# Optimization experiments

Measured on AMD Instinct MI355X. Metric: run time of the kernel, lower is better.

## Reference

```python
import jax, jax.numpy as jnp
import numpy as np

DIM, E, K = 256, 8, 2
B, D, H, W = 1, 32, 32, 32
EPS = 1e-5


def setup_inputs() -> dict:
    key = jax.random.key(0)
    ks = jax.random.split(key, 16)
    nrm = lambda k, s, sc=0.02: jax.random.normal(k, s, jnp.float32) * sc
    def resblock_params(k):
        k1, k2, k3, k4 = jax.random.split(k, 4)
        return dict(
            c1w=nrm(k1, (DIM, DIM, 3, 3, 3)), c1b=jnp.zeros((DIM,), jnp.float32),
            g1=jax.random.uniform(k2, (DIM,), jnp.float32, 0.5, 1.5), be1=jnp.zeros((DIM,), jnp.float32),
            c2w=nrm(k3, (DIM, DIM, 3, 3, 3)), c2b=jnp.zeros((DIM,), jnp.float32),
            g2=jax.random.uniform(k4, (DIM,), jnp.float32, 0.5, 1.5), be2=jnp.zeros((DIM,), jnp.float32),
        )
    p1 = resblock_params(ks[5])
    p2 = resblock_params(ks[6])
    return {
        "x": jax.random.normal(ks[0], (B, DIM, D, H, W), jnp.float32),
        "wg": nrm(ks[1], (DIM, E)),
        "w1": nrm(ks[2], (E, DIM, DIM)), "b1": jnp.zeros((E, DIM), jnp.float32),
        "w2": nrm(ks[3], (E, DIM, DIM)), "b2": jnp.zeros((E, DIM), jnp.float32),
        "r1_c1w": p1["c1w"], "r1_c1b": p1["c1b"], "r1_g1": p1["g1"], "r1_be1": p1["be1"],
        "r1_c2w": p1["c2w"], "r1_c2b": p1["c2b"], "r1_g2": p1["g2"], "r1_be2": p1["be2"],
        "r2_c1w": p2["c1w"], "r2_c1b": p2["c1b"], "r2_g1": p2["g1"], "r2_be1": p2["be1"],
        "r2_c2w": p2["c2w"], "r2_c2b": p2["c2b"], "r2_g2": p2["g2"], "r2_be2": p2["be2"],
        "c8w": nrm(ks[4], (DIM, DIM, 1, 1, 1)), "c8b": jnp.zeros((DIM,), jnp.float32),
    }


def conv3d(x, w, b, pad):
    y = jax.lax.conv_general_dilated(
        x, w, window_strides=(1, 1, 1), padding=[(pad, pad)] * 3,
        dimension_numbers=("NCDHW", "OIDHW", "NCDHW"))
    return y + b[None, :, None, None, None]


def batchnorm(x, g, b):
    m = x.mean(axis=(0, 2, 3, 4), keepdims=True)
    v = x.var(axis=(0, 2, 3, 4), keepdims=True)
    return g[None, :, None, None, None] * (x - m) * jax.lax.rsqrt(v + EPS) + b[None, :, None, None, None]


def unet_res_block(x, c1w, c1b, g1, be1, c2w, c2b, g2, be2):
    out = jax.nn.leaky_relu(batchnorm(conv3d(x, c1w, c1b, 1), g1, be1), 0.01)
    out = batchnorm(conv3d(out, c2w, c2b, 1), g2, be2)
    return jax.nn.leaky_relu(out + x, 0.01)  # identity shortcut (in==out ch, stride 1)


def mom_block(x, wg, w1, b1, w2, b2):
    Bb, C, Dd, Hh, Ww = x.shape
    tokens = x.transpose(0, 2, 3, 4, 1).reshape(-1, C)  # [T, C]
    T = tokens.shape[0]
    probs = jax.nn.softmax(tokens @ wg, axis=-1)          # [T, E]
    vals, idx = jax.lax.top_k(probs, K)                   # [T, K]
    wts = vals / vals.sum(-1, keepdims=True)
    gates = jnp.zeros((T, E), probs.dtype).at[jnp.arange(T)[:, None], idx].set(wts)
    # dense expert MLPs (math-equivalent to gather/dispatch/combine)
    h = jax.nn.gelu(jnp.einsum("tc,ech->eth", tokens, w1) + b1[:, None, :])
    eo = jnp.einsum("eth,ehc->etc", h, w2) + b2[:, None, :]
    moe = jnp.einsum("te,etc->tc", gates, eo)             # [T, C]
    # switch-style load-balancing auxiliary loss
    density = (gates > 0).astype(probs.dtype).mean(0)     # fraction of tokens per expert
    density_proxy = probs.mean(0)
    aux = (density * density_proxy).sum() * E
    out = x + moe.reshape(Bb, Dd, Hh, Ww, C).transpose(0, 4, 1, 2, 3)
    return out, aux


def reference(x, wg, w1, b1, w2, b2,
              r1_c1w, r1_c1b, r1_g1, r1_be1, r1_c2w, r1_c2b, r1_g2, r1_be2,
              r2_c1w, r2_c1b, r2_g1, r2_be1, r2_c2w, r2_c2b, r2_g2, r2_be2,
              c8w, c8b):
    xm, aux = mom_block(x, wg, w1, b1, w2, b2)
    res = unet_res_block(xm, r1_c1w, r1_c1b, r1_g1, r1_be1, r1_c2w, r1_c2b, r1_g2, r1_be2)
    res = unet_res_block(res, r2_c1w, r2_c1b, r2_g1, r2_be1, r2_c2w, r2_c2b, r2_g2, r2_be2)
    out = xm + conv3d(res, c8w, c8b, 0)  # Dropout3d is identity at eval
    return out, aux
```

## Files before the change

### kernel.cpp

```cpp
#include <hip/hip_runtime.h>
#include <stdint.h>

typedef __attribute__((ext_vector_type(8))) short short8;
typedef __attribute__((ext_vector_type(4))) float f32x4;
typedef unsigned short u16;
typedef unsigned int u32;
typedef unsigned long long u64;

#define WS_TOK   0ull
#define WS_XT    16777216ull
#define WS_XMCT  50331648ull
#define WS_GATES 83886080ull
#define WS_H     84934656ull
#define WS_P1    135266304ull
#define WS_P2    155389952ull
#define WS_Y     175513600ull
#define WS_R2    209068032ull
#define WS_WRB   225845248ull
#define WS_W1P   240001024ull
#define WS_W2P   241049600ull
#define WS_C8P   242098176ull
#define WS_PART  242229248ull
#define WS_SF    243277824ull
#define WS_AUXP  243279872ull

#define WS_PERM  (WS_H + 0x00000ull)
#define WS_TBL   (WS_H + 0x60000ull)
#define WS_META  (WS_H + 0x70000ull)
#define WS_BCNT  (WS_H + 0x80000ull)
#define WS_BOFF  (WS_H + 0x90000ull)
#define WS_SEL   (WS_H + 0x100000ull)

__device__ __forceinline__ u16 f2bf(float f) {
  u32 x = __float_as_uint(f);
  u32 r = x + 0x7fffu + ((x >> 16) & 1u);
  return (u16)(r >> 16);
}
__device__ __forceinline__ float bf2f(u32 u) { return __uint_as_float(u << 16); }

__global__ void trans_in_k(const float* __restrict__ x, float* __restrict__ xt,
                           u16* __restrict__ tok) {
  __shared__ float ld[64][65];
  int tt = blockIdx.x, cc = blockIdx.y, tid = threadIdx.x;
#pragma unroll
  for (int k = 0; k < 16; ++k) {
    int idx = tid + k * 256;
    int cl = idx >> 6, j = idx & 63;
    ld[cl][j] = x[(size_t)(cc * 64 + cl) * 32768 + tt * 64 + j];
  }
  __syncthreads();
#pragma unroll
  for (int k = 0; k < 16; ++k) {
    int idx = tid + k * 256;
    int tl = idx >> 6, cl = idx & 63;
    float v = ld[cl][tl];
    size_t o = (size_t)(tt * 64 + tl) * 256 + cc * 64 + cl;
    xt[o] = v;
    tok[o] = f2bf(v);
  }
}

__global__ void pack_rb_k(const float* __restrict__ w0, const float* __restrict__ w1,
                          const float* __restrict__ w2, const float* __restrict__ w3,
                          u16* __restrict__ out) {
  __shared__ float ld[6912];
  int conv = blockIdx.x >> 8, blk = blockIdx.x & 255, tid = threadIdx.x;
  const float* src = conv == 0 ? w0 : conv == 1 ? w1 : conv == 2 ? w2 : w3;
  size_t base = (size_t)blk * 256 * 27;
#pragma unroll
  for (int k = 0; k < 27; ++k) ld[tid + k * 256] = src[base + tid + k * 256];
  __syncthreads();
  u16* dst = out + (size_t)conv * 27 * 65536;
  int n = blk * 256 + tid;
#pragma unroll
  for (int tap = 0; tap < 27; ++tap)
    dst[(size_t)tap * 65536 + n] = f2bf(ld[tid * 27 + tap]);
}

__global__ void pack_tr_k(const float* __restrict__ w1, const float* __restrict__ w2,
                          u16* __restrict__ w1p, u16* __restrict__ w2p) {
  __shared__ float ld[64][65];
  int m = blockIdx.y, tile = blockIdx.x, tid = threadIdx.x;
  const float* src = (m < 8) ? (w1 + (size_t)m * 65536) : (w2 + (size_t)(m - 8) * 65536);
  u16* dst = (m < 8) ? (w1p + (size_t)m * 65536) : (w2p + (size_t)(m - 8) * 65536);
  int r0 = (tile >> 2) * 64, c0 = (tile & 3) * 64;
#pragma unroll
  for (int k = 0; k < 16; ++k) {
    int idx = tid + k * 256;
    int rr = idx >> 6, cc = idx & 63;
    ld[rr][cc] = src[(size_t)(r0 + rr) * 256 + c0 + cc];
  }
  __syncthreads();
#pragma unroll
  for (int k = 0; k < 16; ++k) {
    int idx = tid + k * 256;
    int cc = idx >> 6, rr = idx & 63;
    dst[(size_t)(c0 + cc) * 256 + r0 + rr] = f2bf(ld[rr][cc]);
  }
}

__global__ void cvt_k(const float* __restrict__ in, u16* __restrict__ out, int n) {
  int i = blockIdx.x * 256 + threadIdx.x;
  if (i < n) out[i] = f2bf(in[i]);
}

__global__ void halo_k(u16* __restrict__ P1, u16* __restrict__ P2) {
  int gid = blockIdx.x * 256 + threadIdx.x;
  int r = gid >> 5, o = (gid & 31) << 3;
  if (r >= 39304) return;
  int d = r / 1156, rem = r - d * 1156, h = rem / 34, w = rem - h * 34;
  if (d >= 1 && d <= 32 && h >= 1 && h <= 32 && w >= 1 && w <= 32) return;
  uint4 z = {0u, 0u, 0u, 0u};
  *(uint4*)(P1 + (size_t)r * 256 + o) = z;
  *(uint4*)(P2 + (size_t)r * 256 + o) = z;
}

__global__ void gate_k(const float* __restrict__ xt, const float* __restrict__ wg,
                       float* __restrict__ gw, u32* __restrict__ sel,
                       u32* __restrict__ blk_cnt, float* __restrict__ auxp) {
  __shared__ float wgs[2048];
  __shared__ float ax[4][16];
  __shared__ u32 bc[4][8];
  int tid = threadIdx.x;
#pragma unroll
  for (int k = 0; k < 8; ++k) wgs[tid + k * 256] = wg[tid + k * 256];
  __syncthreads();
  int t = blockIdx.x * 256 + tid;
  int lane = tid & 63, wv = tid >> 6;
  float l[8] = {0, 0, 0, 0, 0, 0, 0, 0};
  const float* xr = xt + (size_t)t * 256;
  for (int c = 0; c < 256; c += 4) {
    float4 xv = *(const float4*)(xr + c);
#pragma unroll
    for (int e = 0; e < 8; ++e)
      l[e] += xv.x * wgs[c * 8 + e] + xv.y * wgs[(c + 1) * 8 + e] +
              xv.z * wgs[(c + 2) * 8 + e] + xv.w * wgs[(c + 3) * 8 + e];
  }
  float mx = l[0];
#pragma unroll
  for (int e = 1; e < 8; ++e) mx = fmaxf(mx, l[e]);
  float p[8], sum = 0.f;
#pragma unroll
  for (int e = 0; e < 8; ++e) { p[e] = __expf(l[e] - mx); sum += p[e]; }
  float inv = 1.0f / sum;
#pragma unroll
  for (int e = 0; e < 8; ++e) p[e] *= inv;
  int i0 = 0; float v0 = p[0];
#pragma unroll
  for (int e = 1; e < 8; ++e) if (p[e] > v0) { v0 = p[e]; i0 = e; }
  int i1 = -1; float v1 = -1.0f;
#pragma unroll
  for (int e = 0; e < 8; ++e) if (e != i0 && p[e] > v1) { v1 = p[e]; i1 = e; }
  float wsum = v0 + v1;
  gw[t * 2] = v0 / wsum;
  gw[t * 2 + 1] = v1 / wsum;
  sel[t] = (u32)i0 | ((u32)i1 << 4);
  u64 mm[8];
#pragma unroll
  for (int e = 0; e < 8; ++e) mm[e] = __ballot(i0 == e || i1 == e);
  if (lane == 0) {
#pragma unroll
    for (int e = 0; e < 8; ++e) bc[wv][e] = (u32)__popcll(mm[e]);
  }
#pragma unroll
  for (int e = 0; e < 8; ++e) {
    float ps = p[e];
    float cn = (e == i0 || e == i1) ? 1.0f : 0.0f;
    for (int o = 32; o; o >>= 1) { ps += __shfl_down(ps, o); cn += __shfl_down(cn, o); }
    if (lane == 0) { ax[wv][e] = ps; ax[wv][8 + e] = cn; }
  }
  __syncthreads();
  if (tid < 16)
    auxp[blockIdx.x * 16 + tid] = ax[0][tid] + ax[1][tid] + ax[2][tid] + ax[3][tid];
  if (tid < 8)
    blk_cnt[blockIdx.x * 8 + tid] = bc[0][tid] + bc[1][tid] + bc[2][tid] + bc[3][tid];
}

__global__ void aux_k(const float* __restrict__ auxp, float* __restrict__ out) {
  __shared__ float s[16];
  int i = threadIdx.x;
  if (i < 16) {
    float a = 0;
    for (int b = 0; b < 128; ++b) a += auxp[b * 16 + i];
    s[i] = a;
  }
  __syncthreads();
  if (i == 0) {
    float r = 0;
    for (int e = 0; e < 8; ++e)
      r += (s[8 + e] * (1.0f / 32768.0f)) * (s[e] * (1.0f / 32768.0f));
    out[0] = r * 8.0f;
  }
}

__global__ void scan_k(const u32* __restrict__ blk_cnt, u32* __restrict__ blkoff,
                       u32* __restrict__ tbl, u32* __restrict__ meta,
                       u32* __restrict__ perm) {
  __shared__ u32 tot[8], base[8], nck[8], cbase[8];
  int tid = threadIdx.x;
  if (tid < 8) {
    u32 run = 0;
    for (int b = 0; b < 128; ++b) {
      blkoff[b * 8 + tid] = run;
      run += blk_cnt[b * 8 + tid];
    }
    tot[tid] = run;
  }
  __syncthreads();
  if (tid == 0) {
    u32 acc = 0, c = 0;
    for (int e = 0; e < 8; ++e) {
      base[e] = acc;
      u32 nc = (tot[e] + 127) >> 7;
      nck[e] = nc;
      cbase[e] = c;
      acc += nc << 7;
      c += nc;
    }
    meta[0] = c;
  }
  __syncthreads();
  for (int i = tid; i < 1024; i += 256) blkoff[i] += base[i & 7];
  if (tid < 8) {
    for (u32 k = 0; k < nck[tid]; ++k)
      tbl[cbase[tid] + k] = ((base[tid] + (k << 7)) << 4) | (u32)tid;
    for (u32 sl = base[tid] + tot[tid]; sl < base[tid] + (nck[tid] << 7); ++sl)
      perm[sl] = 0;
  }
}

__global__ void scatter_k(const u32* __restrict__ sel, const u32* __restrict__ blkoff,
                          u32* __restrict__ perm, u32* __restrict__ tpos) {
  __shared__ u32 wcnt[4][8];
  int tid = threadIdx.x, b = blockIdx.x;
  int lane = tid & 63, wv = tid >> 6;
  int t = b * 256 + tid;
  u32 s = sel[t];
  int i0 = s & 15, i1 = (s >> 4) & 15;
  u64 mm[8];
#pragma unroll
  for (int e = 0; e < 8; ++e) mm[e] = __ballot(i0 == e || i1 == e);
  if (lane == 0) {
#pragma unroll
    for (int e = 0; e < 8; ++e) wcnt[wv][e] = (u32)__popcll(mm[e]);
  }
  __syncthreads();
  u64 lt = (1ull << lane) - 1ull;
#pragma unroll
  for (int e = 0; e < 8; ++e) {
    bool is0 = (i0 == e), is1 = (i1 == e);
    if (is0 || is1) {
      u32 woff = 0;
#pragma unroll
      for (int w = 0; w < 4; ++w)
        if (w < wv) woff += wcnt[w][e];
      u32 pos = blkoff[b * 8 + e] + woff + (u32)__popcll(mm[e] & lt);
      perm[pos] = (u32)t;
      tpos[t * 2 + (is0 ? 0 : 1)] = pos;
    }
  }
}

__global__ __launch_bounds__(512, 2) void moe_gemm_k(
    const u16* __restrict__ tok, const u32* __restrict__ perm,
    const u32* __restrict__ tbl, const u32* __restrict__ meta,
    const u16* __restrict__ w1p, const u16* __restrict__ w2p,
    const float* __restrict__ b1, const float* __restrict__ b2,
    u16* __restrict__ eo) {
  __shared__ __attribute__((aligned(16))) unsigned char smem[163840];
  const int bid = blockIdx.x;
  if ((u32)bid >= meta[0]) return;
  const u32 ent = tbl[bid];
  const int e = (int)(ent & 15u);
  const int slot0 = (int)(ent >> 4);
  const int tid = threadIdx.x;
  const int lane = tid & 63;
  const int wv = tid >> 6;
  const int wr = (wv >> 2) * 64;
  const int wc = (wv & 3) * 64;
  const int fq = lane >> 4, fr = lane & 15;
  const u16* w1e = w1p + e * 65536;
  const u16* w2e = w2p + e * 65536;

#pragma unroll
  for (int it = 0; it < 8; ++it) {
    int s = tid + it * 512;
    int r = s >> 5, seg = s & 31;
    int cole = ((seg >> 3) << 6) + (((seg & 7) ^ (r & 7)) << 3);
    u32 rowtok = perm[slot0 + r];
    __builtin_amdgcn_global_load_lds(
        (const __attribute__((address_space(1))) u32*)(tok + (size_t)rowtok * 256 + cole),
        (__attribute__((address_space(3))) u32*)(smem + s * 16), 16, 0, 0);
  }

  f32x4 acc1[4][4];
#pragma unroll
  for (int mc = 0; mc < 4; ++mc)
#pragma unroll
    for (int nt = 0; nt < 4; ++nt) acc1[mc][nt] = (f32x4){0.f, 0.f, 0.f, 0.f};

#pragma unroll 1
  for (int kc = 0; kc < 4; ++kc) {
#pragma unroll
    for (int it = 0; it < 4; ++it) {
      int s = tid + it * 512;
      int r = s >> 3;
      int sub = (s & 7) ^ (r & 7);
      __builtin_amdgcn_global_load_lds(
          (const __attribute__((address_space(1))) u32*)(w1e + (size_t)r * 256 + kc * 64 + sub * 8),
          (__attribute__((address_space(3))) u32*)(smem + 65536 + s * 16), 16, 0, 0);
    }
    __syncthreads();
#pragma unroll
    for (int khf = 0; khf < 2; ++khf) {
      short8 af1[4], bt[4];
#pragma unroll
      for (int mc = 0; mc < 4; ++mc) {
        int row = wc + mc * 16 + fr;
        int p = (khf * 4 + fq) ^ (row & 7);
        af1[mc] = *(const short8*)(smem + 65536 + row * 128 + p * 16);
      }
#pragma unroll
      for (int nt = 0; nt < 4; ++nt) {
        int row = wr + nt * 16 + fr;
        int p = (khf * 4 + fq) ^ (row & 7);
        bt[nt] = *(const short8*)(smem + row * 512 + kc * 128 + p * 16);
      }
#pragma unroll
      for (int mc = 0; mc < 4; ++mc)
#pragma unroll
        for (int nt = 0; nt < 4; ++nt)
          acc1[mc][nt] = __builtin_amdgcn_mfma_f32_16x16x32_bf16(af1[mc], bt[nt], acc1[mc][nt], 0, 0, 0);
    }
    __syncthreads();
  }

#pragma unroll
  for (int mc = 0; mc < 4; ++mc) {
    int k0 = wc + mc * 16 + fq * 4;
    float4 bv = *(const float4*)(b1 + e * 256 + k0);
#pragma unroll
    for (int nt = 0; nt < 4; ++nt) {
      int t = wr + nt * 16 + fr;
      u64 pk = 0;
#pragma unroll
      for (int j = 0; j < 4; ++j) {
        float v = acc1[mc][nt][j] + ((const float*)&bv)[j];
        float u = 1.5957691216057308f * (v + 0.044715f * v * v * v);
        float g = v / (1.0f + __expf(-u));
        pk |= (u64)f2bf(g) << (16 * j);
      }
      *(u64*)(smem + 98304 + t * 512 + ((k0 * 2) ^ ((t & 7) << 4))) = pk;
    }
  }

  f32x4 acc2[4][4];
#pragma unroll
  for (int m = 0; m < 4; ++m)
#pragma unroll
    for (int n = 0; n < 4; ++n) acc2[m][n] = (f32x4){0.f, 0.f, 0.f, 0.f};

#pragma unroll 1
  for (int kc = 0; kc < 4; ++kc) {
#pragma unroll
    for (int it = 0; it < 4; ++it) {
      int s = tid + it * 512;
      int r = s >> 3;
      int sub = (s & 7) ^ (r & 7);
      __builtin_amdgcn_global_load_lds(
          (const __attribute__((address_space(1))) u32*)(w2e + (size_t)r * 256 + kc * 64 + sub * 8),
          (__attribute__((address_space(3))) u32*)(smem + 65536 + s * 16), 16, 0, 0);
    }
    __syncthreads();
#pragma unroll
    for (int khf = 0; khf < 2; ++khf) {
      short8 af[4], bb[4];
#pragma unroll
      for (int m = 0; m < 4; ++m) {
        int row = wr + m * 16 + fr;
        int col = (kc * 128 + (khf * 4 + fq) * 16) ^ ((row & 7) << 4);
        af[m] = *(const short8*)(smem + 98304 + row * 512 + col);
      }
#pragma unroll
      for (int n = 0; n < 4; ++n) {
        int row = wc + n * 16 + fr;
        int p = (khf * 4 + fq) ^ (row & 7);
        bb[n] = *(const short8*)(smem + 65536 + row * 128 + p * 16);
      }
#pragma unroll
      for (int m = 0; m < 4; ++m)
#pragma unroll
        for (int n = 0; n < 4; ++n)
          acc2[m][n] = __builtin_amdgcn_mfma_f32_16x16x32_bf16(af[m], bb[n], acc2[m][n], 0, 0, 0);
    }
    __syncthreads();
  }

  float bs2[4];
#pragma unroll
  for (int n = 0; n < 4; ++n) bs2[n] = b2[e * 256 + wc + n * 16 + fr];
#pragma unroll
  for (int m = 0; m < 4; ++m)
#pragma unroll
    for (int j = 0; j < 4; ++j) {
      int rowslot = slot0 + wr + m * 16 + fq * 4 + j;
      u16* er = eo + (size_t)rowslot * 256 + wc;
#pragma unroll
      for (int n = 0; n < 4; ++n) er[n * 16 + fr] = f2bf(acc2[m][n][j] + bs2[n]);
    }
}

__global__ void combine_k(float* __restrict__ xt, const u16* __restrict__ eo,
                          const float* __restrict__ gw, const u32* __restrict__ tpos,
                          float* __restrict__ xmct, u16* __restrict__ pad) {
  __shared__ float ld[64][65];
  __shared__ u32 pp[64][2];
  __shared__ float gg[64][2];
  int tt = blockIdx.x, cc = blockIdx.y, tid = threadIdx.x;
  if (tid < 128) {
    int tl = tid >> 1, s = tid & 1;
    int t = tt * 64 + tl;
    pp[tl][s] = tpos[t * 2 + s];
    gg[tl][s] = gw[t * 2 + s];
  }
  __syncthreads();
#pragma unroll
  for (int k = 0; k < 16; ++k) {
    int idx = tid + k * 256;
    int tl = idx >> 6, cl = idx & 63;
    int c = cc * 64 + cl;
    size_t o = (size_t)(tt * 64 + tl) * 256 + c;
    float e0 = bf2f(eo[(size_t)pp[tl][0] * 256 + c]);
    float e1 = bf2f(eo[(size_t)pp[tl][1] * 256 + c]);
    float v = xt[o] + gg[tl][0] * e0 + gg[tl][1] * e1;
    xt[o] = v;
    ld[tl][cl] = v;
    int t = tt * 64 + tl;
    int d = t >> 10, h = (t >> 5) & 31, w = t & 31;
    int prow = (d + 1) * 1156 + (h + 1) * 34 + (w + 1);
    pad[(size_t)prow * 256 + c] = f2bf(v);
  }
  __syncthreads();
#pragma unroll
  for (int k = 0; k < 16; ++k) {
    int idx = tid + k * 256;
    int cl = idx >> 6, tl = idx & 63;
    xmct[(size_t)(cc * 64 + cl) * 32768 + tt * 64 + tl] = ld[tl][cl];
  }
}

__global__ __launch_bounds__(512, 1) void conv_k(
    const u16* __restrict__ P, const u16* __restrict__ W,
    const float* __restrict__ bias, u16* __restrict__ y,
    float* __restrict__ part) {
  __shared__ __attribute__((aligned(16))) unsigned char smem[147456];
  const int tid = threadIdx.x;
  const int bx = blockIdx.x;
  const int ttile = (bx & 7) * 32 + (bx >> 3);
  const int lane = tid & 63;
  const int wv = tid >> 6;
  const int wr = (wv >> 2) << 6;
  const int wc = (wv & 3) << 6;
  const int fq = lane >> 4, fr = lane & 15;
  const int dd = ttile >> 3, h0 = (ttile & 7) << 2;

  int goffA[2];
#pragma unroll
  for (int it = 0; it < 2; ++it) {
    int s = tid + it * 512;
    int r = s >> 3, c = s & 7;
    int base = dd * 1156 + (h0 + (r >> 5)) * 34 + (r & 31);
    goffA[it] = base * 256 + ((c ^ (r & 7)) << 3);
  }
  int goffB[4];
#pragma unroll
  for (int it = 0; it < 4; ++it) {
    int s = tid + it * 512;
    int r = s >> 3, c = s & 7;
    goffB[it] = r * 256 + ((c ^ (r & 7)) << 3);
  }

  f32x4 acc[4][4];
#pragma unroll
  for (int m = 0; m < 4; ++m)
#pragma unroll
    for (int n = 0; n < 4; ++n) acc[m][n] = (f32x4){0.f, 0.f, 0.f, 0.f};

#define CONV_STAGE(s2, half)                                                        \
  {                                                                                 \
    int tap_ = (s2) >> 2, kc_ = (s2) & 3;                                           \
    int aofs_ = ((tap_ / 9) * 1156 + ((tap_ / 3) % 3) * 34 + (tap_ % 3)) * 256 +    \
                kc_ * 64;                                                           \
    int bofs_ = tap_ * 65536 + kc_ * 64;                                            \
    unsigned char* sb_ = smem + ((s2) % 3) * 49152;                                 \
    if ((half) == 0) {                                                              \
      __builtin_amdgcn_global_load_lds(                                             \
          (const __attribute__((address_space(1))) u32*)(P + aofs_ + goffA[0]),     \
          (__attribute__((address_space(3))) u32*)(sb_ + tid * 16), 16, 0, 0);      \
      __builtin_amdgcn_global_load_lds(                                             \
          (const __attribute__((address_space(1))) u32*)(P + aofs_ + goffA[1]),     \
          (__attribute__((address_space(3))) u32*)(sb_ + (tid + 512) * 16), 16, 0, 0); \
      __builtin_amdgcn_global_load_lds(                                             \
          (const __attribute__((address_space(1))) u32*)(W + bofs_ + goffB[0]),     \
          (__attribute__((address_space(3))) u32*)(sb_ + 16384 + tid * 16), 16, 0, 0); \
    } else {                                                                        \
      __builtin_amdgcn_global_load_lds(                                             \
          (const __attribute__((address_space(1))) u32*)(W + bofs_ + goffB[1]),     \
          (__attribute__((address_space(3))) u32*)(sb_ + 16384 + (tid + 512) * 16), \
          16, 0, 0);                                                                \
      __builtin_amdgcn_global_load_lds(                                             \
          (const __attribute__((address_space(1))) u32*)(W + bofs_ + goffB[2]),     \
          (__attribute__((address_space(3))) u32*)(sb_ + 16384 + (tid + 1024) * 16),\
          16, 0, 0);                                                                \
      __builtin_amdgcn_global_load_lds(                                             \
          (const __attribute__((address_space(1))) u32*)(W + bofs_ + goffB[3]),     \
          (__attribute__((address_space(3))) u32*)(sb_ + 16384 + (tid + 1536) * 16),\
          16, 0, 0);                                                                \
    }                                                                               \
  }

  CONV_STAGE(0, 0); CONV_STAGE(0, 1);
  CONV_STAGE(1, 0); CONV_STAGE(1, 1);
  asm volatile("s_waitcnt vmcnt(6)" ::: "memory");
  __builtin_amdgcn_s_barrier();

#pragma unroll 1
  for (int s = 0; s < 108; ++s) {
    const unsigned char* sb = smem + (s % 3) * 49152;
    const bool doStage = (s < 106);
#pragma unroll
    for (int khf = 0; khf < 2; ++khf) {
      short8 af[4], bb[4];
#pragma unroll
      for (int m = 0; m < 4; ++m) {
        int row = wr + m * 16 + fr;
        int p = (khf * 4 + fq) ^ (row & 7);
        af[m] = *(const short8*)(sb + row * 128 + p * 16);
      }
#pragma unroll
      for (int n = 0; n < 4; ++n) {
        int row = wc + n * 16 + fr;
        int p = (khf * 4 + fq) ^ (row & 7);
        bb[n] = *(const short8*)(sb + 16384 + row * 128 + p * 16);
      }
      if (doStage) CONV_STAGE(s + 2, khf);
      __builtin_amdgcn_s_barrier();
      __builtin_amdgcn_s_setprio(1);
#pragma unroll
      for (int m = 0; m < 4; ++m)
#pragma unroll
        for (int n = 0; n < 4; ++n)
          acc[m][n] = __builtin_amdgcn_mfma_f32_16x16x32_bf16(af[m], bb[n], acc[m][n], 0, 0, 0);
      __builtin_amdgcn_s_setprio(0);
      if (khf == 0) __builtin_amdgcn_s_barrier();
    }
    if (doStage)
      asm volatile("s_waitcnt vmcnt(6)" ::: "memory");
    else
      asm volatile("s_waitcnt vmcnt(0)" ::: "memory");
    __builtin_amdgcn_s_barrier();
  }
#undef CONV_STAGE

  float bs[4];
#pragma unroll
  for (int n = 0; n < 4; ++n) bs[n] = bias[wc + n * 16 + fr];

  float sn[4] = {0, 0, 0, 0}, qn[4] = {0, 0, 0, 0};
#pragma unroll
  for (int m = 0; m < 4; ++m) {
#pragma unroll
    for (int j = 0; j < 4; ++j) {
      int t = ttile * 128 + wr + m * 16 + fq * 4 + j;
      u16* yr = y + (size_t)t * 256 + wc;
#pragma unroll
      for (int n = 0; n < 4; ++n) {
        float v = acc[m][n][j] + bs[n];
        yr[n * 16 + fr] = f2bf(v);
        sn[n] += v;
        qn[n] += v * v;
      }
    }
  }
#pragma unroll
  for (int n = 0; n < 4; ++n) {
    float s = sn[n], q = qn[n];
    s += __shfl_xor(s, 16); s += __shfl_xor(s, 32);
    q += __shfl_xor(q, 16); q += __shfl_xor(q, 32);
    if (lane < 16) {
      int pi = (ttile * 2 + (wv >> 2)) * 256 + wc + n * 16 + fr;
      part[pi] = s;
      part[131072 + pi] = q;
    }
  }
}

__global__ __launch_bounds__(256, 2) void final_k(
    const u16* __restrict__ A, const u16* __restrict__ Bw,
    const float* __restrict__ bias, float* __restrict__ outF,
    const float* __restrict__ xmct) {
  __shared__ __attribute__((aligned(16))) unsigned char smem[65536];
  const int tid = threadIdx.x;
  const int ttile = blockIdx.x;
  const int ctile = blockIdx.y;
  const int lane = tid & 63;
  const int wv = tid >> 6;
  const int wr = (wv >> 1) << 6;
  const int wc = (wv & 1) << 6;
  const int fq = lane >> 4;
  const int fr = lane & 15;

  int aoff[4], boff[4];
#pragma unroll
  for (int it = 0; it < 4; ++it) {
    int s = tid + it * 256;
    int r = s >> 3;
    int lsg = (s & 7) ^ (r & 7);
    aoff[it] = (ttile * 128 + r) * 256 + lsg * 8;
    boff[it] = (ctile * 128 + r) * 256 + lsg * 8;
  }

  f32x4 acc[4][4];
#pragma unroll
  for (int m = 0; m < 4; ++m)
#pragma unroll
    for (int n = 0; n < 4; ++n) acc[m][n] = (f32x4){0.f, 0.f, 0.f, 0.f};

  auto stage = [&](int kc, int buf) {
    const u16* Ak = A + kc * 64;
    const u16* Bk = Bw + kc * 64;
    unsigned char* sb = smem + buf * 32768;
#pragma unroll
    for (int it = 0; it < 4; ++it) {
      __builtin_amdgcn_global_load_lds(
          (const __attribute__((address_space(1))) u32*)(Ak + aoff[it]),
          (__attribute__((address_space(3))) u32*)(sb + (tid + it * 256) * 16),
          16, 0, 0);
      __builtin_amdgcn_global_load_lds(
          (const __attribute__((address_space(1))) u32*)(Bk + boff[it]),
          (__attribute__((address_space(3))) u32*)(sb + 16384 + (tid + it * 256) * 16),
          16, 0, 0);
    }
  };
  auto compute = [&](int buf) {
    unsigned char* sb = smem + buf * 32768;
#pragma unroll
    for (int khf = 0; khf < 2; ++khf) {
      short8 af[4], bb[4];
#pragma unroll
      for (int m = 0; m < 4; ++m) {
        int row = wr + m * 16 + fr;
        int p = (khf * 4 + fq) ^ (row & 7);
        af[m] = *(const short8*)(sb + row * 128 + p * 16);
      }
#pragma unroll
      for (int n = 0; n < 4; ++n) {
        int row = wc + n * 16 + fr;
        int p = (khf * 4 + fq) ^ (row & 7);
        bb[n] = *(const short8*)(sb + 16384 + row * 128 + p * 16);
      }
#pragma unroll
      for (int m = 0; m < 4; ++m)
#pragma unroll
        for (int n = 0; n < 4; ++n)
          acc[m][n] = __builtin_amdgcn_mfma_f32_16x16x32_bf16(af[m], bb[n], acc[m][n], 0, 0, 0);
    }
  };

  stage(0, 0);
  asm volatile("s_waitcnt vmcnt(0)" ::: "memory");
  __builtin_amdgcn_s_barrier();
  int cur = 0;
#pragma unroll 1
  for (int s = 0; s < 4; ++s) {
    if (s + 1 < 4) stage(s + 1, cur ^ 1);
    compute(cur);
    asm volatile("s_waitcnt vmcnt(0)" ::: "memory");
    __builtin_amdgcn_s_barrier();
    cur ^= 1;
  }

  float bs[4];
#pragma unroll
  for (int n = 0; n < 4; ++n) bs[n] = bias[ctile * 128 + wc + n * 16 + fr];

#pragma unroll
  for (int m = 0; m < 4; ++m) {
    int trow = ttile * 128 + wr + m * 16 + fq * 4;
#pragma unroll
    for (int n = 0; n < 4; ++n) {
      int oc = ctile * 128 + wc + n * 16 + fr;
      size_t o = (size_t)oc * 32768 + trow;
      float4 xv = *(const float4*)(xmct + o);
      float4 w;
      w.x = acc[m][n][0] + bs[n] + xv.x;
      w.y = acc[m][n][1] + bs[n] + xv.y;
      w.z = acc[m][n][2] + bs[n] + xv.z;
      w.w = acc[m][n][3] + bs[n] + xv.w;
      *(float4*)(outF + o) = w;
    }
  }
}

__global__ void stats2_k(const float* __restrict__ part, const float* __restrict__ g,
                         const float* __restrict__ be, float* __restrict__ sf) {
  __shared__ float sred[4][256], qred[4][256];
  int tid = threadIdx.x;
  int c = tid & 255, qd = tid >> 8;
  float s = 0, q = 0;
  for (int b = qd * 128; b < qd * 128 + 128; ++b) {
    s += part[b * 256 + c];
    q += part[131072 + b * 256 + c];
  }
  sred[qd][c] = s;
  qred[qd][c] = q;
  __syncthreads();
  if (qd == 0) {
    s = sred[0][c] + sred[1][c] + sred[2][c] + sred[3][c];
    q = qred[0][c] + qred[1][c] + qred[2][c] + qred[3][c];
    float mean = s * (1.0f / 32768.0f);
    float var = q * (1.0f / 32768.0f) - mean * mean;
    float a = g[c] * rsqrtf(var + 1e-5f);
    sf[c] = a;
    sf[256 + c] = be[c] - mean * a;
  }
}

template <int V>
__global__ void bn_k(const u16* __restrict__ y, const float* __restrict__ sf,
                     const float* __restrict__ skip, u16* __restrict__ pad,
                     float* __restrict__ f32o, u16* __restrict__ bfo) {
  int gid = blockIdx.x * 256 + threadIdx.x;
  int t = gid >> 5, c0 = (gid & 31) << 3;
  size_t base = (size_t)t * 256 + c0;
  float v[8];
  uint4 yv = *(const uint4*)(y + base);
  v[0] = bf2f(yv.x & 0xffffu); v[1] = bf2f(yv.x >> 16);
  v[2] = bf2f(yv.y & 0xffffu); v[3] = bf2f(yv.y >> 16);
  v[4] = bf2f(yv.z & 0xffffu); v[5] = bf2f(yv.z >> 16);
  v[6] = bf2f(yv.w & 0xffffu); v[7] = bf2f(yv.w >> 16);
  const float4* ap = (const float4*)(sf + c0);
  float4 a0 = ap[0], a1 = ap[1];
  const float4* shp = (const float4*)(sf + 256 + c0);
  float4 s0 = shp[0], s1 = shp[1];
  v[0] = a0.x * v[0] + s0.x; v[1] = a0.y * v[1] + s0.y;
  v[2] = a0.z * v[2] + s0.z; v[3] = a0.w * v[3] + s0.w;
  v[4] = a1.x * v[4] + s1.x; v[5] = a1.y * v[5] + s1.y;
  v[6] = a1.z * v[6] + s1.z; v[7] = a1.w * v[7] + s1.w;
  if (V >= 1) {
    const float4* kp = (const float4*)(skip + base);
    float4 k0 = kp[0], k1 = kp[1];
    v[0] += k0.x; v[1] += k0.y; v[2] += k0.z; v[3] += k0.w;
    v[4] += k1.x; v[5] += k1.y; v[6] += k1.z; v[7] += k1.w;
  }
#pragma unroll
  for (int i = 0; i < 8; ++i) v[i] = v[i] > 0.0f ? v[i] : 0.01f * v[i];
  if (V <= 1) {
    int d = t >> 10, h = (t >> 5) & 31, w = t & 31;
    int prow = (d + 1) * 1156 + (h + 1) * 34 + (w + 1);
    uint4 pk;
    pk.x = (u32)f2bf(v[0]) | ((u32)f2bf(v[1]) << 16);
    pk.y = (u32)f2bf(v[2]) | ((u32)f2bf(v[3]) << 16);
    pk.z = (u32)f2bf(v[4]) | ((u32)f2bf(v[5]) << 16);
    pk.w = (u32)f2bf(v[6]) | ((u32)f2bf(v[7]) << 16);
    *(uint4*)(pad + (size_t)prow * 256 + c0) = pk;
  }
  if (V == 1) {
    float4 o0 = {v[0], v[1], v[2], v[3]}, o1 = {v[4], v[5], v[6], v[7]};
    float4* fp = (float4*)(f32o + base);
    fp[0] = o0; fp[1] = o1;
  }
  if (V == 2) {
    uint4 pk;
    pk.x = (u32)f2bf(v[0]) | ((u32)f2bf(v[1]) << 16);
    pk.y = (u32)f2bf(v[2]) | ((u32)f2bf(v[3]) << 16);
    pk.z = (u32)f2bf(v[4]) | ((u32)f2bf(v[5]) << 16);
    pk.w = (u32)f2bf(v[6]) | ((u32)f2bf(v[7]) << 16);
    *(uint4*)(bfo + base) = pk;
  }
}

extern "C" void kernel_launch(void* const* d_in, const int* in_sizes, int n_in,
                              void* d_out, int out_size, void* d_ws, size_t ws_size,
                              hipStream_t stream) {
  (void)in_sizes; (void)n_in; (void)out_size; (void)ws_size;
  const float* x  = (const float*)d_in[0];
  const float* wg = (const float*)d_in[1];
  const float* w1 = (const float*)d_in[2];
  const float* b1 = (const float*)d_in[3];
  const float* w2 = (const float*)d_in[4];
  const float* b2 = (const float*)d_in[5];

  char* ws = (char*)d_ws;
  u16* tok    = (u16*)(ws + WS_TOK);
  float* xt   = (float*)(ws + WS_XT);
  float* xmct = (float*)(ws + WS_XMCT);
  float* gw   = (float*)(ws + WS_GATES);
  u32* tpos   = (u32*)(ws + WS_GATES + 0x80000ull);
  u32* perm   = (u32*)(ws + WS_PERM);
  u32* tbl    = (u32*)(ws + WS_TBL);
  u32* meta   = (u32*)(ws + WS_META);
  u32* bcnt   = (u32*)(ws + WS_BCNT);
  u32* boff   = (u32*)(ws + WS_BOFF);
  u32* selb   = (u32*)(ws + WS_SEL);
  u16* P1     = (u16*)(ws + WS_P1);
  u16* P2     = (u16*)(ws + WS_P2);
  u16* ybuf   = (u16*)(ws + WS_Y);
  u16* eo     = (u16*)(ws + WS_Y);
  u16* r2b    = (u16*)(ws + WS_R2);
  u16* wrb    = (u16*)(ws + WS_WRB);
  u16* w1p    = (u16*)(ws + WS_W1P);
  u16* w2p    = (u16*)(ws + WS_W2P);
  u16* c8p    = (u16*)(ws + WS_C8P);
  float* part = (float*)(ws + WS_PART);
  float* sf   = (float*)(ws + WS_SF);
  float* auxp = (float*)(ws + WS_AUXP);
  float* outp = (float*)d_out;

  halo_k<<<4913, 256, 0, stream>>>(P1, P2);
  trans_in_k<<<dim3(512, 4), 256, 0, stream>>>(x, xt, tok);
  pack_rb_k<<<1024, 256, 0, stream>>>((const float*)d_in[6], (const float*)d_in[10],
                                      (const float*)d_in[14], (const float*)d_in[18], wrb);
  pack_tr_k<<<dim3(16, 16), 256, 0, stream>>>(w1, w2, w1p, w2p);
  cvt_k<<<256, 256, 0, stream>>>((const float*)d_in[22], c8p, 65536);

  gate_k<<<128, 256, 0, stream>>>(xt, wg, gw, selb, bcnt, auxp);
  scan_k<<<1, 256, 0, stream>>>(bcnt, boff, tbl, meta, perm);
  scatter_k<<<128, 256, 0, stream>>>(selb, boff, perm, tpos);
  moe_gemm_k<<<520, 512, 0, stream>>>(tok, perm, tbl, meta, w1p, w2p, b1, b2, eo);
  combine_k<<<dim3(512, 4), 256, 0, stream>>>(xt, eo, gw, tpos, xmct, P1);

  conv_k<<<256, 512, 0, stream>>>(P1, wrb + 0 * 1769472, (const float*)d_in[7], ybuf, part);
  stats2_k<<<1, 1024, 0, stream>>>(part, (const float*)d_in[8], (const float*)d_in[9], sf);
  bn_k<0><<<4096, 256, 0, stream>>>(ybuf, sf, nullptr, P2, nullptr, nullptr);
  conv_k<<<256, 512, 0, stream>>>(P2, wrb + 1 * 1769472, (const float*)d_in[11], ybuf, part);
  stats2_k<<<1, 1024, 0, stream>>>(part, (const float*)d_in[12], (const float*)d_in[13], sf);
  bn_k<1><<<4096, 256, 0, stream>>>(ybuf, sf, xt, P1, xt, nullptr);

  conv_k<<<256, 512, 0, stream>>>(P1, wrb + 2 * 1769472, (const float*)d_in[15], ybuf, part);
  stats2_k<<<1, 1024, 0, stream>>>(part, (const float*)d_in[16], (const float*)d_in[17], sf);
  bn_k<0><<<4096, 256, 0, stream>>>(ybuf, sf, nullptr, P2, nullptr, nullptr);
  conv_k<<<256, 512, 0, stream>>>(P2, wrb + 3 * 1769472, (const float*)d_in[19], ybuf, part);
  stats2_k<<<1, 1024, 0, stream>>>(part, (const float*)d_in[20], (const float*)d_in[21], sf);
  bn_k<2><<<4096, 256, 0, stream>>>(ybuf, sf, xt, nullptr, nullptr, r2b);

  final_k<<<dim3(256, 2), 256, 0, stream>>>(r2b, c8p, (const float*)d_in[23], outp, xmct);
  aux_k<<<1, 64, 0, stream>>>(auxp, outp + 8388608);
}
```

Measured before the change: 737.9 us.

## Double-buffer MoE weight loads, simplify conv pipeline, parallelize BN stats, gate from raw input

The MoE GEMM now double-buffers its expert-weight chunks in LDS and prefetches the next chunk while computing the current one. It also reuses the token region for the hidden activations, cutting LDS from 160KB to 128KB. The conv kernel's staged-load macro becomes lambdas that issue each stage's loads all at once, dropping the split-half staging, the mid-loop barriers and the setprio hints. stats2 runs across 16 blocks instead of one. The gate kernel reads the channel-major input directly, so it no longer depends on the transpose kernel. The conv scheduling change could lose the overlap the interleaved barriers gave, and the gate's strided reads may coalesce differently.

```diff
diff --git a/kernel.cpp b/kernel.cpp
--- a/kernel.cpp
+++ b/kernel.cpp
@@ -115,7 +115,7 @@
   *(uint4*)(P2 + (size_t)r * 256 + o) = z;
 }
 
-__global__ void gate_k(const float* __restrict__ xt, const float* __restrict__ wg,
+__global__ void gate_k(const float* __restrict__ x, const float* __restrict__ wg,
                        float* __restrict__ gw, u32* __restrict__ sel,
                        u32* __restrict__ blk_cnt, float* __restrict__ auxp) {
   __shared__ float wgs[2048];
@@ -128,13 +128,11 @@
   int t = blockIdx.x * 256 + tid;
   int lane = tid & 63, wv = tid >> 6;
   float l[8] = {0, 0, 0, 0, 0, 0, 0, 0};
-  const float* xr = xt + (size_t)t * 256;
-  for (int c = 0; c < 256; c += 4) {
-    float4 xv = *(const float4*)(xr + c);
-#pragma unroll
-    for (int e = 0; e < 8; ++e)
-      l[e] += xv.x * wgs[c * 8 + e] + xv.y * wgs[(c + 1) * 8 + e] +
-              xv.z * wgs[(c + 2) * 8 + e] + xv.w * wgs[(c + 3) * 8 + e];
+#pragma unroll 4
+  for (int c = 0; c < 256; ++c) {
+    float xv = x[(size_t)c * 32768 + t];
+#pragma unroll
+    for (int e = 0; e < 8; ++e) l[e] += xv * wgs[c * 8 + e];
   }
   float mx = l[0];
 #pragma unroll
@@ -267,7 +265,7 @@
     const u16* __restrict__ w1p, const u16* __restrict__ w2p,
     const float* __restrict__ b1, const float* __restrict__ b2,
     u16* __restrict__ eo) {
-  __shared__ __attribute__((aligned(16))) unsigned char smem[163840];
+  __shared__ __attribute__((aligned(16))) unsigned char smem[131072];
   const int bid = blockIdx.x;
   if ((u32)bid >= meta[0]) return;
   const u32 ent = tbl[bid];
@@ -282,6 +280,14 @@
   const u16* w1e = w1p + e * 65536;
   const u16* w2e = w2p + e * 65536;
 
+  int woff[4];
+#pragma unroll
+  for (int it = 0; it < 4; ++it) {
+    int s = tid + it * 512;
+    int r = s >> 3;
+    woff[it] = r * 256 + (((s & 7) ^ (r & 7)) << 3);
+  }
+
 #pragma unroll
   for (int it = 0; it < 8; ++it) {
     int s = tid + it * 512;
@@ -292,6 +298,13 @@
         (const __attribute__((address_space(1))) u32*)(tok + (size_t)rowtok * 256 + cole),
         (__attribute__((address_space(3))) u32*)(smem + s * 16), 16, 0, 0);
   }
+#pragma unroll
+  for (int it = 0; it < 4; ++it)
+    __builtin_amdgcn_global_load_lds(
+        (const __attribute__((address_space(1))) u32*)(w1e + woff[it]),
+        (__attribute__((address_space(3))) u32*)(smem + 65536 + (tid + it * 512) * 16),
+        16, 0, 0);
+  __syncthreads();
 
   f32x4 acc1[4][4];
 #pragma unroll
@@ -301,16 +314,15 @@
 
 #pragma unroll 1
   for (int kc = 0; kc < 4; ++kc) {
-#pragma unroll
-    for (int it = 0; it < 4; ++it) {
-      int s = tid + it * 512;
-      int r = s >> 3;
-      int sub = (s & 7) ^ (r & 7);
+    const u16* nw = (kc < 3) ? (w1e + (kc + 1) * 64) : w2e;
+    unsigned char* nb = smem + 65536 + (((kc + 1) & 1) * 32768);
+#pragma unroll
+    for (int it = 0; it < 4; ++it)
       __builtin_amdgcn_global_load_lds(
-          (const __attribute__((address_space(1))) u32*)(w1e + (size_t)r * 256 + kc * 64 + sub * 8),
-          (__attribute__((address_space(3))) u32*)(smem + 65536 + s * 16), 16, 0, 0);
-    }
-    __syncthreads();
+          (const __attribute__((address_space(1))) u32*)(nw + woff[it]),
+          (__attribute__((address_space(3))) u32*)(nb + (tid + it * 512) * 16),
+          16, 0, 0);
+    const unsigned char* wb = smem + 65536 + ((kc & 1) * 32768);
 #pragma unroll
     for (int khf = 0; khf < 2; ++khf) {
       short8 af1[4], bt[4];
@@ -318,7 +330,7 @@
       for (int mc = 0; mc < 4; ++mc) {
         int row = wc + mc * 16 + fr;
         int p = (khf * 4 + fq) ^ (row & 7);
-        af1[mc] = *(const short8*)(smem + 65536 + row * 128 + p * 16);
+        af1[mc] = *(const short8*)(wb + row * 128 + p * 16);
       }
 #pragma unroll
       for (int nt = 0; nt < 4; ++nt) {
@@ -350,9 +362,10 @@
         float g = v / (1.0f + __expf(-u));
         pk |= (u64)f2bf(g) << (16 * j);
       }
-      *(u64*)(smem + 98304 + t * 512 + ((k0 * 2) ^ ((t & 7) << 4))) = pk;
-    }
-  }
+      *(u64*)(smem + t * 512 + ((k0 * 2) ^ ((t & 7) << 4))) = pk;
+    }
+  }
+  __syncthreads();
 
   f32x4 acc2[4][4];
 #pragma unroll
@@ -362,16 +375,17 @@
 
 #pragma unroll 1
   for (int kc = 0; kc < 4; ++kc) {
-#pragma unroll
-    for (int it = 0; it < 4; ++it) {
-      int s = tid + it * 512;
-      int r = s >> 3;
-      int sub = (s & 7) ^ (r & 7);
-      __builtin_amdgcn_global_load_lds(
-          (const __attribute__((address_space(1))) u32*)(w2e + (size_t)r * 256 + kc * 64 + sub * 8),
-          (__attribute__((address_space(3))) u32*)(smem + 65536 + s * 16), 16, 0, 0);
-    }
-    __syncthreads();
+    if (kc < 3) {
+      unsigned char* nb = smem + 65536 + (((kc + 1) & 1) * 32768);
+      const u16* nw = w2e + (kc + 1) * 64;
+#pragma unroll
+      for (int it = 0; it < 4; ++it)
+        __builtin_amdgcn_global_load_lds(
+            (const __attribute__((address_space(1))) u32*)(nw + woff[it]),
+            (__attribute__((address_space(3))) u32*)(nb + (tid + it * 512) * 16),
+            16, 0, 0);
+    }
+    const unsigned char* wb = smem + 65536 + ((kc & 1) * 32768);
 #pragma unroll
     for (int khf = 0; khf < 2; ++khf) {
       short8 af[4], bb[4];
@@ -379,13 +393,13 @@
       for (int m = 0; m < 4; ++m) {
         int row = wr + m * 16 + fr;
         int col = (kc * 128 + (khf * 4 + fq) * 16) ^ ((row & 7) << 4);
-        af[m] = *(const short8*)(smem + 98304 + row * 512 + col);
+        af[m] = *(const short8*)(smem + row * 512 + col);
       }
 #pragma unroll
       for (int n = 0; n < 4; ++n) {
         int row = wc + n * 16 + fr;
         int p = (khf * 4 + fq) ^ (row & 7);
-        bb[n] = *(const short8*)(smem + 65536 + row * 128 + p * 16);
+        bb[n] = *(const short8*)(wb + row * 128 + p * 16);
       }
 #pragma unroll
       for (int m = 0; m < 4; ++m)
@@ -464,20 +478,20 @@
   const int fq = lane >> 4, fr = lane & 15;
   const int dd = ttile >> 3, h0 = (ttile & 7) << 2;
 
-  int goffA[2];
+  int aoff[2];
 #pragma unroll
   for (int it = 0; it < 2; ++it) {
     int s = tid + it * 512;
     int r = s >> 3, c = s & 7;
     int base = dd * 1156 + (h0 + (r >> 5)) * 34 + (r & 31);
-    goffA[it] = base * 256 + ((c ^ (r & 7)) << 3);
-  }
-  int goffB[4];
+    aoff[it] = base * 256 + ((c ^ (r & 7)) << 3);
+  }
+  int boff[4];
 #pragma unroll
   for (int it = 0; it < 4; ++it) {
     int s = tid + it * 512;
     int r = s >> 3, c = s & 7;
-    goffB[it] = r * 256 + ((c ^ (r & 7)) << 3);
+    boff[it] = r * 256 + ((c ^ (r & 7)) << 3);
   }
 
   f32x4 acc[4][4];
@@ -486,48 +500,26 @@
 #pragma unroll
     for (int n = 0; n < 4; ++n) acc[m][n] = (f32x4){0.f, 0.f, 0.f, 0.f};
 
-#define CONV_STAGE(s2, half)                                                        \
-  {                                                                                 \
-    int tap_ = (s2) >> 2, kc_ = (s2) & 3;                                           \
-    int aofs_ = ((tap_ / 9) * 1156 + ((tap_ / 3) % 3) * 34 + (tap_ % 3)) * 256 +    \
-                kc_ * 64;                                                           \
-    int bofs_ = tap_ * 65536 + kc_ * 64;                                            \
-    unsigned char* sb_ = smem + ((s2) % 3) * 49152;                                 \
-    if ((half) == 0) {                                                              \
-      __builtin_amdgcn_global_load_lds(                                             \
-          (const __attribute__((address_space(1))) u32*)(P + aofs_ + goffA[0]),     \
-          (__attribute__((address_space(3))) u32*)(sb_ + tid * 16), 16, 0, 0);      \
-      __builtin_amdgcn_global_load_lds(                                             \
-          (const __attribute__((address_space(1))) u32*)(P + aofs_ + goffA[1]),     \
-          (__attribute__((address_space(3))) u32*)(sb_ + (tid + 512) * 16), 16, 0, 0); \
-      __builtin_amdgcn_global_load_lds(                                             \
-          (const __attribute__((address_space(1))) u32*)(W + bofs_ + goffB[0]),     \
-          (__attribute__((address_space(3))) u32*)(sb_ + 16384 + tid * 16), 16, 0, 0); \
-    } else {                                                                        \
-      __builtin_amdgcn_global_load_lds(                                             \
-          (const __attribute__((address_space(1))) u32*)(W + bofs_ + goffB[1]),     \
-          (__attribute__((address_space(3))) u32*)(sb_ + 16384 + (tid + 512) * 16), \
-          16, 0, 0);                                                                \
-      __builtin_amdgcn_global_load_lds(                                             \
-          (const __attribute__((address_space(1))) u32*)(W + bofs_ + goffB[2]),     \
-          (__attribute__((address_space(3))) u32*)(sb_ + 16384 + (tid + 1024) * 16),\
-          16, 0, 0);                                                                \
-      __builtin_amdgcn_global_load_lds(                                             \
-          (const __attribute__((address_space(1))) u32*)(W + bofs_ + goffB[3]),     \
-          (__attribute__((address_space(3))) u32*)(sb_ + 16384 + (tid + 1536) * 16),\
-          16, 0, 0);                                                                \
-    }                                                                               \
-  }
-
-  CONV_STAGE(0, 0); CONV_STAGE(0, 1);
-  CONV_STAGE(1, 0); CONV_STAGE(1, 1);
-  asm volatile("s_waitcnt vmcnt(6)" ::: "memory");
-  __builtin_amdgcn_s_barrier();
-
-#pragma unroll 1
-  for (int s = 0; s < 108; ++s) {
-    const unsigned char* sb = smem + (s % 3) * 49152;
-    const bool doStage = (s < 106);
+  auto stage = [&](int s, int buf) {
+    int tap = s >> 2, kc = s & 3;
+    int aofs = ((tap / 9) * 1156 + ((tap / 3) % 3) * 34 + (tap % 3)) * 256 + kc * 64;
+    int bofs = tap * 65536 + kc * 64;
+    unsigned char* sb = smem + buf * 49152;
+#pragma unroll
+    for (int it = 0; it < 2; ++it)
+      __builtin_amdgcn_global_load_lds(
+          (const __attribute__((address_space(1))) u32*)(P + aofs + aoff[it]),
+          (__attribute__((address_space(3))) u32*)(sb + (tid + it * 512) * 16),
+          16, 0, 0);
+#pragma unroll
+    for (int it = 0; it < 4; ++it)
+      __builtin_amdgcn_global_load_lds(
+          (const __attribute__((address_space(1))) u32*)(W + bofs + boff[it]),
+          (__attribute__((address_space(3))) u32*)(sb + 16384 + (tid + it * 512) * 16),
+          16, 0, 0);
+  };
+  auto compute = [&](int buf) {
+    const unsigned char* sb = smem + buf * 49152;
 #pragma unroll
     for (int khf = 0; khf < 2; ++khf) {
       short8 af[4], bb[4];
@@ -543,24 +535,29 @@
         int p = (khf * 4 + fq) ^ (row & 7);
         bb[n] = *(const short8*)(sb + 16384 + row * 128 + p * 16);
       }
-      if (doStage) CONV_STAGE(s + 2, khf);
-      __builtin_amdgcn_s_barrier();
-      __builtin_amdgcn_s_setprio(1);
 #pragma unroll
       for (int m = 0; m < 4; ++m)
 #pragma unroll
         for (int n = 0; n < 4; ++n)
           acc[m][n] = __builtin_amdgcn_mfma_f32_16x16x32_bf16(af[m], bb[n], acc[m][n], 0, 0, 0);
-      __builtin_amdgcn_s_setprio(0);
-      if (khf == 0) __builtin_amdgcn_s_barrier();
-    }
-    if (doStage)
+    }
+  };
+
+  stage(0, 0);
+  stage(1, 1);
+  asm volatile("s_waitcnt vmcnt(6)" ::: "memory");
+  __builtin_amdgcn_s_barrier();
+
+#pragma unroll 1
+  for (int s = 0; s < 108; ++s) {
+    if (s < 106) stage(s + 2, (s + 2) % 3);
+    compute(s % 3);
+    if (s < 106)
       asm volatile("s_waitcnt vmcnt(6)" ::: "memory");
     else
       asm volatile("s_waitcnt vmcnt(0)" ::: "memory");
     __builtin_amdgcn_s_barrier();
   }
-#undef CONV_STAGE
 
   float bs[4];
 #pragma unroll
@@ -643,7 +640,7 @@
     }
   };
   auto compute = [&](int buf) {
-    unsigned char* sb = smem + buf * 32768;
+    const unsigned char* sb = smem + buf * 32768;
 #pragma unroll
     for (int khf = 0; khf < 2; ++khf) {
       short8 af[4], bb[4];
@@ -704,20 +701,22 @@
 
 __global__ void stats2_k(const float* __restrict__ part, const float* __restrict__ g,
                          const float* __restrict__ be, float* __restrict__ sf) {
-  __shared__ float sred[4][256], qred[4][256];
+  __shared__ float sred[16][16], qred[16][16];
   int tid = threadIdx.x;
-  int c = tid & 255, qd = tid >> 8;
+  int cl = tid & 15, ch = tid >> 4;
+  int c = blockIdx.x * 16 + cl;
   float s = 0, q = 0;
-  for (int b = qd * 128; b < qd * 128 + 128; ++b) {
+  for (int b = ch * 32; b < ch * 32 + 32; ++b) {
     s += part[b * 256 + c];
     q += part[131072 + b * 256 + c];
   }
-  sred[qd][c] = s;
-  qred[qd][c] = q;
-  __syncthreads();
-  if (qd == 0) {
-    s = sred[0][c] + sred[1][c] + sred[2][c] + sred[3][c];
-    q = qred[0][c] + qred[1][c] + qred[2][c] + qred[3][c];
+  sred[ch][cl] = s;
+  qred[ch][cl] = q;
+  __syncthreads();
+  if (ch == 0) {
+    s = 0; q = 0;
+#pragma unroll
+    for (int k = 0; k < 16; ++k) { s += sred[k][cl]; q += qred[k][cl]; }
     float mean = s * (1.0f / 32768.0f);
     float var = q * (1.0f / 32768.0f) - mean * mean;
     float a = g[c] * rsqrtf(var + 1e-5f);
@@ -818,30 +817,30 @@
   float* outp = (float*)d_out;
 
   halo_k<<<4913, 256, 0, stream>>>(P1, P2);
+  gate_k<<<128, 256, 0, stream>>>(x, wg, gw, selb, bcnt, auxp);
   trans_in_k<<<dim3(512, 4), 256, 0, stream>>>(x, xt, tok);
   pack_rb_k<<<1024, 256, 0, stream>>>((const float*)d_in[6], (const float*)d_in[10],
                                       (const float*)d_in[14], (const float*)d_in[18], wrb);
   pack_tr_k<<<dim3(16, 16), 256, 0, stream>>>(w1, w2, w1p, w2p);
   cvt_k<<<256, 256, 0, stream>>>((const float*)d_in[22], c8p, 65536);
 
-  gate_k<<<128, 256, 0, stream>>>(xt, wg, gw, selb, bcnt, auxp);
   scan_k<<<1, 256, 0, stream>>>(bcnt, boff, tbl, meta, perm);
   scatter_k<<<128, 256, 0, stream>>>(selb, boff, perm, tpos);
   moe_gemm_k<<<520, 512, 0, stream>>>(tok, perm, tbl, meta, w1p, w2p, b1, b2, eo);
   combine_k<<<dim3(512, 4), 256, 0, stream>>>(xt, eo, gw, tpos, xmct, P1);
 
   conv_k<<<256, 512, 0, stream>>>(P1, wrb + 0 * 1769472, (const float*)d_in[7], ybuf, part);
-  stats2_k<<<1, 1024, 0, stream>>>(part, (const float*)d_in[8], (const float*)d_in[9], sf);
+  stats2_k<<<16, 256, 0, stream>>>(part, (const float*)d_in[8], (const float*)d_in[9], sf);
   bn_k<0><<<4096, 256, 0, stream>>>(ybuf, sf, nullptr, P2, nullptr, nullptr);
   conv_k<<<256, 512, 0, stream>>>(P2, wrb + 1 * 1769472, (const float*)d_in[11], ybuf, part);
-  stats2_k<<<1, 1024, 0, stream>>>(part, (const float*)d_in[12], (const float*)d_in[13], sf);
+  stats2_k<<<16, 256, 0, stream>>>(part, (const float*)d_in[12], (const float*)d_in[13], sf);
   bn_k<1><<<4096, 256, 0, stream>>>(ybuf, sf, xt, P1, xt, nullptr);
 
   conv_k<<<256, 512, 0, stream>>>(P1, wrb + 2 * 1769472, (const float*)d_in[15], ybuf, part);
-  stats2_k<<<1, 1024, 0, stream>>>(part, (const float*)d_in[16], (const float*)d_in[17], sf);
+  stats2_k<<<16, 256, 0, stream>>>(part, (const float*)d_in[16], (const float*)d_in[17], sf);
   bn_k<0><<<4096, 256, 0, stream>>>(ybuf, sf, nullptr, P2, nullptr, nullptr);
   conv_k<<<256, 512, 0, stream>>>(P2, wrb + 3 * 1769472, (const float*)d_in[19], ybuf, part);
-  stats2_k<<<1, 1024, 0, stream>>>(part, (const float*)d_in[20], (const float*)d_in[21], sf);
+  stats2_k<<<16, 256, 0, stream>>>(part, (const float*)d_in[20], (const float*)d_in[21], sf);
   bn_k<2><<<4096, 256, 0, stream>>>(ybuf, sf, xt, nullptr, nullptr, r2b);
 
   final_k<<<dim3(256, 2), 256, 0, stream>>>(r2b, c8p, (const float*)d_in[23], outp, xmct);
```

Result: faster. 680.3 us (-7.8%).
